# Kernel optimization log

Measured on AMD Instinct MI355X. Metric: run time of the kernel, lower is better.

## Reference

```python
import jax, jax.numpy as jnp
import numpy as np

B, S, H, NH = 4, 320, 512, 8
DH = H // NH
RAND_S = 320  # weibo randomAttention size
NEG = -1e15


def setup_inputs() -> dict:
    rng = jax.random.key(0)
    ks = jax.random.split(rng, 14)
    s = 0.02
    return {
        "query": jax.random.normal(ks[0], (B, S, H), jnp.float32),
        "key": jax.random.normal(ks[1], (B, S, H), jnp.float32),
        "value": jax.random.normal(ks[2], (B, S, H), jnp.float32),
        "rel_pos_embedding": jax.random.normal(ks[3], (B, S, S, H), jnp.float32),
        "seq_len": jax.random.randint(ks[4], (B,), 1, S + 1),
        "lex_num": 0,
        "Wq": jax.random.normal(ks[5], (H, H), jnp.float32) * s,
        "bq": jax.random.normal(ks[6], (H,), jnp.float32) * s,
        "Wv": jax.random.normal(ks[7], (H, H), jnp.float32) * s,
        "bv": jax.random.normal(ks[8], (H,), jnp.float32) * s,
        "Wr": jax.random.normal(ks[9], (H, H), jnp.float32) * s,
        "br": jax.random.normal(ks[10], (H,), jnp.float32) * s,
        "u": jax.random.normal(ks[11], (NH, DH), jnp.float32) * s,
        "v": jax.random.normal(ks[12], (NH, DH), jnp.float32) * s,
        "rand_attn": jax.random.normal(ks[13], (1, NH, RAND_S, RAND_S), jnp.float32) * s,
    }


def reference(query, key, value, rel_pos_embedding, seq_len, lex_num,
              Wq, bq, Wv, bv, Wr, br, u, v, rand_attn):
    # Linear projections (torch Linear: x @ W.T + b). Note: key is NOT projected.
    q = query @ Wq.T + bq                      # [B,S,H]
    val = value @ Wv.T + bv                    # [B,S,H]
    rel = rel_pos_embedding @ Wr.T + br        # [B,S,S,H]

    # Split heads
    q = q.reshape(B, S, NH, DH).transpose(0, 2, 1, 3)     # [B,NH,S,DH]
    k = key.reshape(B, S, NH, DH).transpose(0, 2, 1, 3)   # [B,NH,S,DH]
    val = val.reshape(B, S, NH, DH).transpose(0, 2, 1, 3) # [B,NH,S,DH]
    rel = rel.reshape(B, S, S, NH, DH)                    # [B,Sq,Sk,NH,DH]

    # A+C: (q + u) k^T
    A_C = jnp.einsum('bhqd,bhkd->bhqk', q + u[None, :, None, :], k)
    # B+D: (q + v) contracted with relative position embeddings
    B_D = jnp.einsum('bhqd,bqkhd->bhqk', q + v[None, :, None, :], rel)

    scores = A_C + B_D + rand_attn[:, :, :S, :S]          # [B,NH,S,S]

    lengths = seq_len + lex_num                           # [B]
    mask = jnp.arange(S)[None, :] < lengths[:, None]      # [B,S] key mask
    scores = jnp.where(mask[:, None, None, :], scores, NEG)

    attn = jax.nn.softmax(scores, axis=-1)                # dropout p=0 -> identity
    out = jnp.einsum('bhqk,bhkd->bhqd', attn, val)        # [B,NH,S,DH]
    return out.transpose(0, 2, 1, 3).reshape(B, S, H)
```

## Files before the change

### kernel.cpp

```cpp
#include <hip/hip_runtime.h>


#define NEGV (-1e15f)

typedef unsigned int u32;

__device__ __forceinline__ void gl_lds16(const float* g, float* l) {
  __builtin_amdgcn_global_load_lds(
      (const __attribute__((address_space(1))) u32*)(g),
      (__attribute__((address_space(3))) u32*)(l), 16, 0, 0);
}

__device__ __forceinline__ float dot4f(const float4 a, const float4 b) {
  return a.x*b.x + a.y*b.y + a.z*b.z + a.w*b.w;
}

__global__ __launch_bounds__(256) void k1_proj(
    const float* __restrict__ query, const float* __restrict__ value,
    const float* __restrict__ Wq, const float* __restrict__ bq,
    const float* __restrict__ Wv, const float* __restrict__ bv,
    const float* __restrict__ u, const float* __restrict__ v,
    float* __restrict__ qu, float* __restrict__ qv, float* __restrict__ valp)
{
  const int rt = blockIdx.x;
  const int ct = blockIdx.y;
  const int which = blockIdx.z;
  const int t = threadIdx.x;
  const int R0 = rt * 16;

  __shared__ float xs[16][516];

  const float* X = which ? value : query;
  const float* W = which ? Wv : Wq;
  const float* bias = which ? bv : bq;

  #pragma unroll
  for (int j = 0; j < 8; ++j) {
    int f4 = t + 256 * j;
    int row = f4 >> 7, c4 = f4 & 127;
    float4 xv = *reinterpret_cast<const float4*>(X + (size_t)(R0 + row) * 512 + c4 * 4);
    *reinterpret_cast<float4*>(&xs[row][c4 * 4]) = xv;
  }
  __syncthreads();

  const int r = t >> 4, clo = t & 15;
  #pragma unroll
  for (int sub = 0; sub < 2; ++sub) {
    const int cb = ct * 128 + sub * 64 + clo * 4;
    float a0 = 0.f, a1 = 0.f, a2 = 0.f, a3 = 0.f;
    const float* w0p = W + (size_t)(cb + 0) * 512;
    const float* w1p = W + (size_t)(cb + 1) * 512;
    const float* w2p = W + (size_t)(cb + 2) * 512;
    const float* w3p = W + (size_t)(cb + 3) * 512;
    #pragma unroll 2
    for (int m4 = 0; m4 < 128; ++m4) {
      float4 x4 = *reinterpret_cast<const float4*>(&xs[r][m4 * 4]);
      float4 w0 = *reinterpret_cast<const float4*>(w0p + m4 * 4);
      float4 w1 = *reinterpret_cast<const float4*>(w1p + m4 * 4);
      float4 w2 = *reinterpret_cast<const float4*>(w2p + m4 * 4);
      float4 w3 = *reinterpret_cast<const float4*>(w3p + m4 * 4);
      a0 += dot4f(x4, w0);
      a1 += dot4f(x4, w1);
      a2 += dot4f(x4, w2);
      a3 += dot4f(x4, w3);
    }
    a0 += bias[cb + 0]; a1 += bias[cb + 1]; a2 += bias[cb + 2]; a3 += bias[cb + 3];
    const size_t ob = (size_t)(R0 + r) * 512 + cb;
    if (which == 0) {
      float4 o1, o2;
      o1.x = a0 + u[cb + 0]; o1.y = a1 + u[cb + 1]; o1.z = a2 + u[cb + 2]; o1.w = a3 + u[cb + 3];
      o2.x = a0 + v[cb + 0]; o2.y = a1 + v[cb + 1]; o2.z = a2 + v[cb + 2]; o2.w = a3 + v[cb + 3];
      *reinterpret_cast<float4*>(qu + ob) = o1;
      *reinterpret_cast<float4*>(qv + ob) = o2;
    } else {
      float4 o; o.x = a0; o.y = a1; o.z = a2; o.w = a3;
      *reinterpret_cast<float4*>(valp + ob) = o;
    }
  }
}

__global__ __launch_bounds__(256, 2) void k4_attn(
    const float* __restrict__ rpe, const float* __restrict__ key,
    const float* __restrict__ Wr, const float* __restrict__ br,
    const float* __restrict__ rand_attn,
    const int* __restrict__ seq_len, const int* __restrict__ lex_num,
    const float* __restrict__ qu, const float* __restrict__ qv,
    const float* __restrict__ valp,
    float* __restrict__ out)
{
  const int q = blockIdx.x;
  const int b = blockIdx.y;
  const int t = threadIdx.x;
  const int w = t >> 6;
  const int lane = t & 63;
  const int row8 = lane >> 3;
  const int chunk = lane & 7;

  __shared__ float bufA[2][16][512];
  __shared__ float sc[8][320];

  const size_t bq = (size_t)b * 320 + q;
  const float* rpe_bq = rpe + bq * 320 * 512;
  float* wscr = &bufA[1][0][0];

  int g[8];
  #pragma unroll
  for (int j = 0; j < 8; ++j) {
    int o = (w * 8 + j) * 1024 + lane * 16;
    int row = o >> 11;
    int ch  = (o >> 8) & 7;
    int win = (o >> 7) & 1;
    int slot = (o >> 4) & 7;
    int i = win * 8 + (slot ^ ((row ^ ch) & 7));
    g[j] = row * 512 + (ch * 16 + i) * 4;
  }

  #pragma unroll
  for (int j = 0; j < 8; ++j)
    gl_lds16(rpe_bq + g[j], &bufA[0][0][0] + (w * 8 + j) * 256);

  const int hh = t >> 5, m = t & 31;
  const float* qv_row = qv + bq * 512 + hh * 64;

  {
    float4 a4[4];
    #pragma unroll
    for (int ii = 0; ii < 4; ++ii) { a4[ii].x = 0.f; a4[ii].y = 0.f; a4[ii].z = 0.f; a4[ii].w = 0.f; }
    const float* wrb = Wr + (size_t)(hh * 64) * 512 + m * 16;
    #pragma unroll 4
    for (int d = 0; d < 64; ++d) {
      float s = qv_row[d];
      const float4* w4 = reinterpret_cast<const float4*>(wrb + (size_t)d * 512);
      #pragma unroll
      for (int ii = 0; ii < 4; ++ii) {
        a4[ii].x += s * w4[ii].x; a4[ii].y += s * w4[ii].y;
        a4[ii].z += s * w4[ii].z; a4[ii].w += s * w4[ii].w;
      }
    }
    #pragma unroll
    for (int ii = 0; ii < 4; ++ii)
      *reinterpret_cast<float4*>(wscr + hh * 512 + m * 16 + ii * 4) = a4[ii];
  }

  float c = 0.f;
  #pragma unroll 8
  for (int d = 0; d < 64; ++d) c += qv_row[d] * br[hh * 64 + d];

  const int len = seq_len[b] + lex_num[0];
  {
    const float* qup = qu + bq * 512 + hh * 64;
    const float* keyb = key + (size_t)b * 320 * 512 + hh * 64;
    const float* rnd_hq = rand_attn + ((size_t)hh * 320 + q) * 320;
    #pragma unroll
    for (int i = 0; i < 10; ++i) {
      const int k = m + 32 * i;
      float val;
      if (k < len) {
        const float* kr = keyb + (size_t)k * 512;
        float a = 0.f;
        #pragma unroll
        for (int ii = 0; ii < 16; ++ii)
          a += dot4f(reinterpret_cast<const float4*>(qup)[ii],
                     reinterpret_cast<const float4*>(kr)[ii]);
        val = a + rnd_hq[k] + c;
      } else {
        val = NEGV;
      }
      sc[hh][k] = val;
    }
  }
  __syncthreads();

  const int h0 = 2 * w, h1 = 2 * w + 1;
  float4 wc0[16], wc1[16];
  #pragma unroll
  for (int i = 0; i < 16; ++i) {
    wc0[i] = *reinterpret_cast<const float4*>(wscr + h0 * 512 + chunk * 64 + i * 4);
    wc1[i] = *reinterpret_cast<const float4*>(wscr + h1 * 512 + chunk * 64 + i * 4);
  }
  __syncthreads();

  const int rc = (row8 ^ chunk) & 7;
  const int Cb0 = row8 * 2048 + chunk * 256 + rc * 16;
  const char* bufbase = reinterpret_cast<const char*>(&bufA[0][0][0]);

  int cb = 0;
  for (int tile = 0; tile < 20; ++tile) {
    if (tile + 1 < 20) {
      const float* src = rpe_bq + (size_t)(tile + 1) * 8192;
      float* dst = &bufA[cb ^ 1][0][0];
      #pragma unroll
      for (int j = 0; j < 8; ++j)
        gl_lds16(src + g[j], dst + (w * 8 + j) * 256);
    }

    const char* bufc = bufbase + cb * 32768;
    #pragma unroll
    for (int pass = 0; pass < 2; ++pass) {
      const int C = Cb0 + pass * 16384;
      float a0 = 0.f, a1 = 0.f;
      #pragma unroll
      for (int i = 0; i < 16; ++i) {
        const float4 r4 = *reinterpret_cast<const float4*>(bufc + (C ^ (i << 4)));
        a0 += dot4f(r4, wc0[i]);
        a1 += dot4f(r4, wc1[i]);
      }
      a0 += __shfl_xor(a0, 1, 8);
      a0 += __shfl_xor(a0, 2, 8);
      a0 += __shfl_xor(a0, 4, 8);
      a1 += __shfl_xor(a1, 1, 8);
      a1 += __shfl_xor(a1, 2, 8);
      a1 += __shfl_xor(a1, 4, 8);
      if (chunk == 0) {
        const int kk = tile * 16 + pass * 8 + row8;
        sc[h0][kk] += a0;
        sc[h1][kk] += a1;
      }
    }
    __syncthreads();
    cb ^= 1;
  }

  {
    float vals[10];
    float mx = -3.0e38f;
    #pragma unroll
    for (int i = 0; i < 10; ++i) { vals[i] = sc[hh][m + 32 * i]; mx = fmaxf(mx, vals[i]); }
    mx = fmaxf(mx, __shfl_xor(mx, 1, 32));
    mx = fmaxf(mx, __shfl_xor(mx, 2, 32));
    mx = fmaxf(mx, __shfl_xor(mx, 4, 32));
    mx = fmaxf(mx, __shfl_xor(mx, 8, 32));
    mx = fmaxf(mx, __shfl_xor(mx, 16, 32));
    float s = 0.f;
    #pragma unroll
    for (int i = 0; i < 10; ++i) { vals[i] = __expf(vals[i] - mx); s += vals[i]; }
    s += __shfl_xor(s, 1, 32);
    s += __shfl_xor(s, 2, 32);
    s += __shfl_xor(s, 4, 32);
    s += __shfl_xor(s, 8, 32);
    s += __shfl_xor(s, 16, 32);
    const float inv = 1.0f / s;
    #pragma unroll
    for (int i = 0; i < 10; ++i) sc[hh][m + 32 * i] = vals[i] * inv;
  }
  __syncthreads();

  {
    const int d2 = m;
    float2 a0; a0.x = 0.f; a0.y = 0.f;
    float2 a1; a1.x = 0.f; a1.y = 0.f;
    const float* vb = valp + (size_t)b * 320 * 512 + hh * 64 + d2 * 2;
    #pragma unroll 4
    for (int k = 0; k < 320; k += 2) {
      float p0 = sc[hh][k], p1 = sc[hh][k + 1];
      float2 v0 = *reinterpret_cast<const float2*>(vb + (size_t)k * 512);
      float2 v1 = *reinterpret_cast<const float2*>(vb + (size_t)(k + 1) * 512);
      a0.x += p0 * v0.x; a0.y += p0 * v0.y;
      a1.x += p1 * v1.x; a1.y += p1 * v1.y;
    }
    float2 o; o.x = a0.x + a1.x; o.y = a0.y + a1.y;
    *reinterpret_cast<float2*>(out + bq * 512 + hh * 64 + d2 * 2) = o;
  }
}

extern "C" void kernel_launch(void* const* d_in, const int* in_sizes, int n_in,
                              void* d_out, int out_size, void* d_ws, size_t ws_size,
                              hipStream_t stream) {
  const float* query = (const float*)d_in[0];
  const float* key   = (const float*)d_in[1];
  const float* value = (const float*)d_in[2];
  const float* rpe   = (const float*)d_in[3];
  const int*   seq_len = (const int*)d_in[4];
  const int*   lex_num = (const int*)d_in[5];
  const float* Wq = (const float*)d_in[6];
  const float* bq = (const float*)d_in[7];
  const float* Wv = (const float*)d_in[8];
  const float* bv = (const float*)d_in[9];
  const float* Wr = (const float*)d_in[10];
  const float* br = (const float*)d_in[11];
  const float* u  = (const float*)d_in[12];
  const float* v  = (const float*)d_in[13];
  const float* rnd = (const float*)d_in[14];

  float* out = (float*)d_out;
  float* ws = (float*)d_ws;
  float* qu    = ws;
  float* qv    = ws + 655360;
  float* valp  = ws + 1310720;

  k1_proj<<<dim3(80, 4, 2), 256, 0, stream>>>(query, value, Wq, bq, Wv, bv, u, v, qu, qv, valp);
  k4_attn<<<dim3(320, 4), 256, 0, stream>>>(rpe, key, Wr, br, rnd, seq_len, lex_num, qu, qv, valp, out);
}
```

Before: 684.5 us.

## Interleave key-score computation into rpe tile loop and remap blocks per XCD

The q·k score pass, which ran as a separate phase before the rel-pos streaming loop, is now split into 16-key chunks. Each chunk is computed inside the tile loop for the next tile, with each key dot product split across two lanes and combined by a shuffle. This overlaps the key loads and FMA work with the rpe tile streaming instead of serializing them. The grid is also flattened and remapped so each XCD handles one half of one batch, which is meant to keep that batch's key, qu and valp data local to one L2. The added per-tile work sits on the barrier-bound loop and may lengthen each iteration.

```diff
diff --git a/kernel.cpp b/kernel.cpp
--- a/kernel.cpp
+++ b/kernel.cpp
@@ -88,8 +88,10 @@
     const float* __restrict__ valp,
     float* __restrict__ out)
 {
-  const int q = blockIdx.x;
-  const int b = blockIdx.y;
+  const int xcd = blockIdx.x & 7;
+  const int idx = blockIdx.x >> 3;
+  const int b = xcd >> 1;
+  const int q = (xcd & 1) * 160 + idx;
   const int t = threadIdx.x;
   const int w = t >> 6;
   const int lane = t & 63;
@@ -147,27 +149,21 @@
   for (int d = 0; d < 64; ++d) c += qv_row[d] * br[hh * 64 + d];
 
   const int len = seq_len[b] + lex_num[0];
+  const float* qup    = qu + bq * 512 + hh * 64 + (m >> 4) * 32;
+  const float* keyb   = key + (size_t)b * 320 * 512 + hh * 64 + (m >> 4) * 32;
+  const float* rnd_hq = rand_attn + ((size_t)hh * 320 + q) * 320;
+
   {
-    const float* qup = qu + bq * 512 + hh * 64;
-    const float* keyb = key + (size_t)b * 320 * 512 + hh * 64;
-    const float* rnd_hq = rand_attn + ((size_t)hh * 320 + q) * 320;
-    #pragma unroll
-    for (int i = 0; i < 10; ++i) {
-      const int k = m + 32 * i;
-      float val;
-      if (k < len) {
-        const float* kr = keyb + (size_t)k * 512;
-        float a = 0.f;
-        #pragma unroll
-        for (int ii = 0; ii < 16; ++ii)
-          a += dot4f(reinterpret_cast<const float4*>(qup)[ii],
-                     reinterpret_cast<const float4*>(kr)[ii]);
-        val = a + rnd_hq[k] + c;
-      } else {
-        val = NEGV;
-      }
-      sc[hh][k] = val;
-    }
+    const int kk = m & 15;
+    float a = 0.f;
+    const float* kr = keyb + (size_t)kk * 512;
+    #pragma unroll
+    for (int ii = 0; ii < 8; ++ii)
+      a += dot4f(reinterpret_cast<const float4*>(qup)[ii],
+                 reinterpret_cast<const float4*>(kr)[ii]);
+    a += __shfl_xor(a, 16, 32);
+    if (m < 16)
+      sc[hh][kk] = (kk < len) ? a + rnd_hq[kk] + c : NEGV;
   }
   __syncthreads();
 
@@ -217,6 +213,20 @@
         sc[h1][kk] += a1;
       }
     }
+
+    if (tile + 1 < 20) {
+      const int kk = (tile + 1) * 16 + (m & 15);
+      float a = 0.f;
+      const float* kr = keyb + (size_t)kk * 512;
+      #pragma unroll
+      for (int ii = 0; ii < 8; ++ii)
+        a += dot4f(reinterpret_cast<const float4*>(qup)[ii],
+                   reinterpret_cast<const float4*>(kr)[ii]);
+      a += __shfl_xor(a, 16, 32);
+      if (m < 16)
+        sc[hh][kk] = (kk < len) ? a + rnd_hq[kk] + c : NEGV;
+    }
+
     __syncthreads();
     cb ^= 1;
   }
@@ -289,5 +299,5 @@
   float* valp  = ws + 1310720;
 
   k1_proj<<<dim3(80, 4, 2), 256, 0, stream>>>(query, value, Wq, bq, Wv, bv, u, v, qu, qv, valp);
-  k4_attn<<<dim3(320, 4), 256, 0, stream>>>(rpe, key, Wr, br, rnd, seq_len, lex_num, qu, qv, valp, out);
-}
+  k4_attn<<<1280, 256, 0, stream>>>(rpe, key, Wr, br, rnd, seq_len, lex_num, qu, qv, valp, out);
+}
```

Result: slower. 713.9 us (+4.3%).
